# Kernel tuning notes

Measured on AMD Instinct MI355X. Metric: run time of the kernel, lower is better.

The kernel has to match this reference:

```python
import jax, jax.numpy as jnp
import numpy as np

NUM_HEADS = 32
NUM_KV_HEADS = 8
HEAD_DIM = 128
SCALE = 1.0 / np.sqrt(HEAD_DIM)
BATCH = 16
MAX_CTX = 2048
NUM_SLOTS = BATCH * MAX_CTX + BATCH  # 32784; last BATCH slots are the write targets


def setup_inputs() -> dict:
    key = jax.random.key(0)
    ks = jax.random.split(key, 8)
    q = jax.random.normal(ks[0], (BATCH, NUM_HEADS, HEAD_DIM), dtype=jnp.float32)
    k = jax.random.normal(ks[1], (BATCH, NUM_KV_HEADS, HEAD_DIM), dtype=jnp.float32)
    v = jax.random.normal(ks[2], (BATCH, NUM_KV_HEADS, HEAD_DIM), dtype=jnp.float32)
    k_cache = jax.random.normal(ks[3], (NUM_SLOTS, NUM_KV_HEADS, HEAD_DIM), dtype=jnp.float32)
    v_cache = jax.random.normal(ks[4], (NUM_SLOTS, NUM_KV_HEADS, HEAD_DIM), dtype=jnp.float32)
    # each decode token writes its new kv into a fresh slot at the end of the pool
    slot_mapping = (BATCH * MAX_CTX + jnp.arange(BATCH)).astype(jnp.int64)
    # sparse-controller-selected active slots per request (paged, irregular)
    active_slots = jax.random.randint(ks[5], (BATCH, MAX_CTX), 0, NUM_SLOTS).astype(jnp.int64)
    # make the current token's slot the last active slot of its own request
    active_slots = active_slots.at[:, -1].set(slot_mapping)
    context_lens = jax.random.randint(ks[6], (BATCH,), 1, MAX_CTX + 1).astype(jnp.int64)
    return {
        "q": q, "k": k, "v": v,
        "k_cache": k_cache, "v_cache": v_cache,
        "slot_mapping": slot_mapping,
        "active_slots": active_slots,
        "context_lens": context_lens,
    }


def _attend(q, k, v, k_cache, v_cache, slot_mapping, active_slots, context_lens):
    # store_kvcache: scatter new k/v into flat slot cache; slot == -1 is skipped
    safe_slots = jnp.where(slot_mapping < 0, NUM_SLOTS, slot_mapping)  # OOB -> dropped
    kc = k_cache.at[safe_slots].set(k, mode="drop")
    vc = v_cache.at[safe_slots].set(v, mode="drop")

    # paged gather of the per-request active KV pages
    K = kc[active_slots]  # [B, L, Hkv, D]
    V = vc[active_slots]  # [B, L, Hkv, D]

    B, H, D = q.shape
    G = H // NUM_KV_HEADS  # GQA group size
    qg = q.reshape(B, NUM_KV_HEADS, G, D)

    # flash-decode stage1+stage2 == numerically-stable softmax attention over active slots
    scores = jnp.einsum("bkgd,blkd->bkgl", qg, K) * SCALE  # [B, Hkv, G, L]
    valid = jnp.arange(active_slots.shape[1])[None, :] < context_lens[:, None]  # [B, L]
    scores = jnp.where(valid[:, None, None, :], scores, jnp.float32(-1e30))
    p = jax.nn.softmax(scores, axis=-1)
    o = jnp.einsum("bkgl,blkd->bkgd", p, V).reshape(B, H, D)
    return o


def reference(q, k, v, k_cache, v_cache, slot_mapping, active_slots, context_lens):
    return _attend(q, k, v, k_cache, v_cache, slot_mapping, active_slots, context_lens)
```

## Files before the change

kernel.cpp:

```cpp
#include <hip/hip_runtime.h>
#include <hip/hip_bf16.h>
#include <float.h>

#define B 16
#define H 32
#define HKV 8
#define G 4
#define D 128
#define LMAX 2048
#define SCALE 0.08838834764831844f

template <int CHUNK>
__global__ __launch_bounds__(64, 3) void attn_partial(
    const float* __restrict__ q,
    const float* __restrict__ kin,
    const float* __restrict__ vin,
    const float* __restrict__ kc,
    const float* __restrict__ vc,
    const int*  __restrict__ slot_mapping,
    const int*  __restrict__ active_slots,
    const int*  __restrict__ context_lens,
    float* __restrict__ part_o,
    float* __restrict__ part_ml)
{
    constexpr int NSPLIT = LMAX / CHUNK;
    const int tid   = threadIdx.x;
    const int split = blockIdx.x % NSPLIT;
    const int h     = (blockIdx.x / NSPLIT) % HKV;
    const int b     = blockIdx.x / (NSPLIT * HKV);

    const int ctx   = context_lens[b];
    const int start = split * CHUNK;
    int nvalid = ctx - start;
    if (nvalid > CHUNK) nvalid = CHUNK;

    const size_t pbase = ((size_t)(b * HKV + h) * NSPLIT + split) * G;

    if (nvalid <= 0) {
        if (tid < G * 2) part_ml[pbase * 2 + tid] = (tid & 1) ? 0.f : -FLT_MAX;
        return;
    }

    __shared__ const float* kp[CHUNK];
    __shared__ const float* vp[CHUNK];
    __shared__ float4 sc4[CHUNK];

    for (int li = tid; li < nvalid; li += 64) {
        const int s = active_slots[b * LMAX + start + li];
        int ov = -1;
#pragma unroll
        for (int j = 0; j < 16; ++j)
            if (slot_mapping[j] == s) ov = j;
        kp[li] = (ov >= 0) ? kin + ((size_t)ov * HKV + h) * D : kc + ((size_t)s * HKV + h) * D;
        vp[li] = (ov >= 0) ? vin + ((size_t)ov * HKV + h) * D : vc + ((size_t)s * HKV + h) * D;
    }

    const int grp   = tid >> 3;
    const int lane8 = tid & 7;

    float4 qv[G][4];
#pragma unroll
    for (int g = 0; g < G; ++g) {
        const float* qp = q + ((size_t)(b * H + h * G + g)) * D;
#pragma unroll
        for (int i = 0; i < 4; ++i) {
            float4 t = *(const float4*)(qp + i * 32 + lane8 * 4);
            qv[g][i] = make_float4(t.x * SCALE, t.y * SCALE, t.z * SCALE, t.w * SCALE);
        }
    }

    constexpr int KIT = CHUNK / 8;
#pragma unroll 2
    for (int it = 0; it < KIT; ++it) {
        const int r  = it * 8 + grp;
        const int rl = (r < nvalid) ? r : nvalid - 1;
        const float* kb = kp[rl];
        float pd0 = 0.f, pd1 = 0.f, pd2 = 0.f, pd3 = 0.f;
#pragma unroll
        for (int j = 0; j < 4; ++j) {
            const float4 kv = *(const float4*)(kb + j * 32 + lane8 * 4);
            pd0 += kv.x * qv[0][j].x + kv.y * qv[0][j].y + kv.z * qv[0][j].z + kv.w * qv[0][j].w;
            pd1 += kv.x * qv[1][j].x + kv.y * qv[1][j].y + kv.z * qv[1][j].z + kv.w * qv[1][j].w;
            pd2 += kv.x * qv[2][j].x + kv.y * qv[2][j].y + kv.z * qv[2][j].z + kv.w * qv[2][j].w;
            pd3 += kv.x * qv[3][j].x + kv.y * qv[3][j].y + kv.z * qv[3][j].z + kv.w * qv[3][j].w;
        }
#pragma unroll
        for (int msk = 1; msk < 8; msk <<= 1) {
            pd0 += __shfl_xor(pd0, msk, 8);
            pd1 += __shfl_xor(pd1, msk, 8);
            pd2 += __shfl_xor(pd2, msk, 8);
            pd3 += __shfl_xor(pd3, msk, 8);
        }
        if (lane8 == 0) sc4[r] = make_float4(pd0, pd1, pd2, pd3);
    }

    {
        constexpr int SR = (CHUNK + 63) / 64;
        float4 s[SR];
#pragma unroll
        for (int k2 = 0; k2 < SR; ++k2) {
            const int l = tid + k2 * 64;
            s[k2] = sc4[l];
            if (l >= nvalid) s[k2] = make_float4(-1e30f, -1e30f, -1e30f, -1e30f);
        }
        float m0 = s[0].x, m1 = s[0].y, m2 = s[0].z, m3 = s[0].w;
#pragma unroll
        for (int k2 = 1; k2 < SR; ++k2) {
            m0 = fmaxf(m0, s[k2].x); m1 = fmaxf(m1, s[k2].y);
            m2 = fmaxf(m2, s[k2].z); m3 = fmaxf(m3, s[k2].w);
        }
#pragma unroll
        for (int msk = 1; msk < 64; msk <<= 1) {
            m0 = fmaxf(m0, __shfl_xor(m0, msk));
            m1 = fmaxf(m1, __shfl_xor(m1, msk));
            m2 = fmaxf(m2, __shfl_xor(m2, msk));
            m3 = fmaxf(m3, __shfl_xor(m3, msk));
        }
        float l0 = 0.f, l1 = 0.f, l2 = 0.f, l3 = 0.f;
#pragma unroll
        for (int k2 = 0; k2 < SR; ++k2) {
            const float4 p = make_float4(__expf(s[k2].x - m0), __expf(s[k2].y - m1),
                                         __expf(s[k2].z - m2), __expf(s[k2].w - m3));
            l0 += p.x; l1 += p.y; l2 += p.z; l3 += p.w;
            sc4[tid + k2 * 64] = p;
        }
#pragma unroll
        for (int msk = 1; msk < 64; msk <<= 1) {
            l0 += __shfl_xor(l0, msk);
            l1 += __shfl_xor(l1, msk);
            l2 += __shfl_xor(l2, msk);
            l3 += __shfl_xor(l3, msk);
        }
        if (tid == 0) {
            *(float4*)&part_ml[pbase * 2 + 0] = make_float4(m0, l0, m1, l1);
            *(float4*)&part_ml[pbase * 2 + 4] = make_float4(m2, l2, m3, l3);
        }
    }

    {
        const int half = tid >> 5;
        const int dl   = tid & 31;
        float4 a0 = {0,0,0,0}, a1 = {0,0,0,0}, a2 = {0,0,0,0}, a3 = {0,0,0,0};
        constexpr int VJ = CHUNK / 2;
#pragma unroll 4
        for (int j = 0; j < VJ; ++j) {
            const int r  = 2 * j + half;
            const int rl = (r < nvalid) ? r : nvalid - 1;
            const float4 vv = *(const float4*)(vp[rl] + dl * 4);
            const float4 p4 = sc4[r];
            a0.x += p4.x * vv.x; a0.y += p4.x * vv.y; a0.z += p4.x * vv.z; a0.w += p4.x * vv.w;
            a1.x += p4.y * vv.x; a1.y += p4.y * vv.y; a1.z += p4.y * vv.z; a1.w += p4.y * vv.w;
            a2.x += p4.z * vv.x; a2.y += p4.z * vv.y; a2.z += p4.z * vv.z; a2.w += p4.z * vv.w;
            a3.x += p4.w * vv.x; a3.y += p4.w * vv.y; a3.z += p4.w * vv.z; a3.w += p4.w * vv.w;
        }
#pragma unroll
        for (int c = 0; c < 4; ++c) {
            ((float*)&a0)[c] += __shfl_xor(((float*)&a0)[c], 32);
            ((float*)&a1)[c] += __shfl_xor(((float*)&a1)[c], 32);
            ((float*)&a2)[c] += __shfl_xor(((float*)&a2)[c], 32);
            ((float*)&a3)[c] += __shfl_xor(((float*)&a3)[c], 32);
        }
        if (half == 0) {
            *(float4*)(part_o + (pbase + 0) * D + dl * 4) = a0;
            *(float4*)(part_o + (pbase + 1) * D + dl * 4) = a1;
        } else {
            *(float4*)(part_o + (pbase + 2) * D + dl * 4) = a2;
            *(float4*)(part_o + (pbase + 3) * D + dl * 4) = a3;
        }
    }
}

__global__ __launch_bounds__(128) void attn_reduce(
    const float* __restrict__ part_o,
    const float* __restrict__ part_ml,
    float* __restrict__ out,
    int nsplit)
{
    const int g = blockIdx.x & 3;
    const int h = (blockIdx.x >> 2) & 7;
    const int b = blockIdx.x >> 5;
    const int d = threadIdx.x;

    __shared__ float mlds[32], llds[32];
    const size_t base = (size_t)(b * HKV + h) * nsplit;

    for (int s = d; s < nsplit; s += 128) {
        mlds[s] = part_ml[((base + s) * G + g) * 2 + 0];
        llds[s] = part_ml[((base + s) * G + g) * 2 + 1];
    }
    __syncthreads();

    float M = -FLT_MAX;
    for (int s = 0; s < nsplit; ++s)
        if (llds[s] > 0.f) M = fmaxf(M, mlds[s]);

    float L = 0.f, acc = 0.f;
    for (int s = 0; s < nsplit; ++s) {
        const float l = llds[s];
        if (l > 0.f) {
            const float e = __expf(mlds[s] - M);
            L += l * e;
            acc += e * part_o[((base + s) * G + g) * D + d];
        }
    }
    out[((size_t)(b * H) + h * G + g) * D + d] = acc / (L > 0.f ? L : 1.f);
}

extern "C" void kernel_launch(void* const* d_in, const int* in_sizes, int n_in,
                              void* d_out, int out_size, void* d_ws, size_t ws_size,
                              hipStream_t stream) {
    const float* q  = (const float*)d_in[0];
    const float* k  = (const float*)d_in[1];
    const float* v  = (const float*)d_in[2];
    const float* kc = (const float*)d_in[3];
    const float* vc = (const float*)d_in[4];
    const int* slot_mapping = (const int*)d_in[5];
    const int* active_slots = (const int*)d_in[6];
    const int* context_lens = (const int*)d_in[7];
    float* out = (float*)d_out;

    const size_t perSplit = (size_t)B * HKV * (G * D + G * 2) * sizeof(float);
    int nsplit = 8;
    if (ws_size >= 32 * perSplit)      nsplit = 32;
    else if (ws_size >= 16 * perSplit) nsplit = 16;

    float* part_o  = (float*)d_ws;
    float* part_ml = part_o + (size_t)B * HKV * nsplit * G * D;

    if (nsplit == 32) {
        attn_partial<64><<<B * HKV * 32, 64, 0, stream>>>(
            q, k, v, kc, vc, slot_mapping, active_slots, context_lens, part_o, part_ml);
    } else if (nsplit == 16) {
        attn_partial<128><<<B * HKV * 16, 64, 0, stream>>>(
            q, k, v, kc, vc, slot_mapping, active_slots, context_lens, part_o, part_ml);
    } else {
        attn_partial<256><<<B * HKV * 8, 64, 0, stream>>>(
            q, k, v, kc, vc, slot_mapping, active_slots, context_lens, part_o, part_ml);
    }
    attn_reduce<<<B * HKV * G, 128, 0, stream>>>(part_o, part_ml, out, nsplit);
}
```

Before: 41.82 us.

## Fuse QK and PV into single-pass online softmax with lazy rescaling

Replaces the three-phase partial kernel (scores to LDS, block softmax, separate PV pass) with one loop in which each 8-lane group loads K and V rows together and keeps an online softmax with a lazy-rescale threshold. The eight group partials are merged through shared memory at the end. The reduce kernel is widened to 256 threads and splits the nsplit loop across two halves. The intent is to overlap K and V gathers and drop the serial phases, at the cost of many more accumulator registers (64 floats of output per thread). The launch-bounds occupancy hint is also removed.

```diff
diff --git a/kernel.cpp b/kernel.cpp
--- a/kernel.cpp
+++ b/kernel.cpp
@@ -9,9 +9,10 @@
 #define D 128
 #define LMAX 2048
 #define SCALE 0.08838834764831844f
+#define THR 8.0f
 
 template <int CHUNK>
-__global__ __launch_bounds__(64, 3) void attn_partial(
+__global__ __launch_bounds__(64) void attn_partial(
     const float* __restrict__ q,
     const float* __restrict__ kin,
     const float* __restrict__ vin,
@@ -43,14 +44,18 @@
 
     __shared__ const float* kp[CHUNK];
     __shared__ const float* vp[CHUNK];
-    __shared__ float4 sc4[CHUNK];
-
+    __shared__ float  red[8][G][D];
+    __shared__ float2 mlred[8][G];
+
+    int smv[16];
+#pragma unroll
+    for (int j = 0; j < 16; ++j) smv[j] = slot_mapping[j];
     for (int li = tid; li < nvalid; li += 64) {
         const int s = active_slots[b * LMAX + start + li];
         int ov = -1;
 #pragma unroll
         for (int j = 0; j < 16; ++j)
-            if (slot_mapping[j] == s) ov = j;
+            if (smv[j] == s) ov = j;
         kp[li] = (ov >= 0) ? kin + ((size_t)ov * HKV + h) * D : kc + ((size_t)s * HKV + h) * D;
         vp[li] = (ov >= 0) ? vin + ((size_t)ov * HKV + h) * D : vc + ((size_t)s * HKV + h) * D;
     }
@@ -63,26 +68,36 @@
     for (int g = 0; g < G; ++g) {
         const float* qp = q + ((size_t)(b * H + h * G + g)) * D;
 #pragma unroll
-        for (int i = 0; i < 4; ++i) {
-            float4 t = *(const float4*)(qp + i * 32 + lane8 * 4);
-            qv[g][i] = make_float4(t.x * SCALE, t.y * SCALE, t.z * SCALE, t.w * SCALE);
-        }
-    }
-
-    constexpr int KIT = CHUNK / 8;
+        for (int j = 0; j < 4; ++j) {
+            float4 t = *(const float4*)(qp + j * 32 + lane8 * 4);
+            qv[g][j] = make_float4(t.x * SCALE, t.y * SCALE, t.z * SCALE, t.w * SCALE);
+        }
+    }
+
+    float m0 = -1e30f, m1 = -1e30f, m2 = -1e30f, m3 = -1e30f;
+    float l0 = 0.f, l1 = 0.f, l2 = 0.f, l3 = 0.f;
+    float4 o0[4] = {}, o1[4] = {}, o2[4] = {}, o3[4] = {};
+
+    constexpr int ITERS = CHUNK / 8;
 #pragma unroll 2
-    for (int it = 0; it < KIT; ++it) {
+    for (int it = 0; it < ITERS; ++it) {
         const int r  = it * 8 + grp;
         const int rl = (r < nvalid) ? r : nvalid - 1;
         const float* kb = kp[rl];
+        const float* vb = vp[rl];
+        float4 kv[4], vv[4];
+#pragma unroll
+        for (int j = 0; j < 4; ++j) kv[j] = *(const float4*)(kb + j * 32 + lane8 * 4);
+#pragma unroll
+        for (int j = 0; j < 4; ++j) vv[j] = *(const float4*)(vb + j * 32 + lane8 * 4);
+
         float pd0 = 0.f, pd1 = 0.f, pd2 = 0.f, pd3 = 0.f;
 #pragma unroll
         for (int j = 0; j < 4; ++j) {
-            const float4 kv = *(const float4*)(kb + j * 32 + lane8 * 4);
-            pd0 += kv.x * qv[0][j].x + kv.y * qv[0][j].y + kv.z * qv[0][j].z + kv.w * qv[0][j].w;
-            pd1 += kv.x * qv[1][j].x + kv.y * qv[1][j].y + kv.z * qv[1][j].z + kv.w * qv[1][j].w;
-            pd2 += kv.x * qv[2][j].x + kv.y * qv[2][j].y + kv.z * qv[2][j].z + kv.w * qv[2][j].w;
-            pd3 += kv.x * qv[3][j].x + kv.y * qv[3][j].y + kv.z * qv[3][j].z + kv.w * qv[3][j].w;
+            pd0 += kv[j].x * qv[0][j].x + kv[j].y * qv[0][j].y + kv[j].z * qv[0][j].z + kv[j].w * qv[0][j].w;
+            pd1 += kv[j].x * qv[1][j].x + kv[j].y * qv[1][j].y + kv[j].z * qv[1][j].z + kv[j].w * qv[1][j].w;
+            pd2 += kv[j].x * qv[2][j].x + kv[j].y * qv[2][j].y + kv[j].z * qv[2][j].z + kv[j].w * qv[2][j].w;
+            pd3 += kv[j].x * qv[3][j].x + kv[j].y * qv[3][j].y + kv[j].z * qv[3][j].z + kv[j].w * qv[3][j].w;
         }
 #pragma unroll
         for (int msk = 1; msk < 8; msk <<= 1) {
@@ -91,86 +106,87 @@
             pd2 += __shfl_xor(pd2, msk, 8);
             pd3 += __shfl_xor(pd3, msk, 8);
         }
-        if (lane8 == 0) sc4[r] = make_float4(pd0, pd1, pd2, pd3);
-    }
-
-    {
-        constexpr int SR = (CHUNK + 63) / 64;
-        float4 s[SR];
-#pragma unroll
-        for (int k2 = 0; k2 < SR; ++k2) {
-            const int l = tid + k2 * 64;
-            s[k2] = sc4[l];
-            if (l >= nvalid) s[k2] = make_float4(-1e30f, -1e30f, -1e30f, -1e30f);
-        }
-        float m0 = s[0].x, m1 = s[0].y, m2 = s[0].z, m3 = s[0].w;
-#pragma unroll
-        for (int k2 = 1; k2 < SR; ++k2) {
-            m0 = fmaxf(m0, s[k2].x); m1 = fmaxf(m1, s[k2].y);
-            m2 = fmaxf(m2, s[k2].z); m3 = fmaxf(m3, s[k2].w);
-        }
-#pragma unroll
-        for (int msk = 1; msk < 64; msk <<= 1) {
-            m0 = fmaxf(m0, __shfl_xor(m0, msk));
-            m1 = fmaxf(m1, __shfl_xor(m1, msk));
-            m2 = fmaxf(m2, __shfl_xor(m2, msk));
-            m3 = fmaxf(m3, __shfl_xor(m3, msk));
-        }
-        float l0 = 0.f, l1 = 0.f, l2 = 0.f, l3 = 0.f;
-#pragma unroll
-        for (int k2 = 0; k2 < SR; ++k2) {
-            const float4 p = make_float4(__expf(s[k2].x - m0), __expf(s[k2].y - m1),
-                                         __expf(s[k2].z - m2), __expf(s[k2].w - m3));
-            l0 += p.x; l1 += p.y; l2 += p.z; l3 += p.w;
-            sc4[tid + k2 * 64] = p;
-        }
-#pragma unroll
-        for (int msk = 1; msk < 64; msk <<= 1) {
-            l0 += __shfl_xor(l0, msk);
-            l1 += __shfl_xor(l1, msk);
-            l2 += __shfl_xor(l2, msk);
-            l3 += __shfl_xor(l3, msk);
-        }
+
+        const bool valid = (r < nvalid);
+        const float s0 = valid ? pd0 : -1e30f;
+        const float s1 = valid ? pd1 : -1e30f;
+        const float s2 = valid ? pd2 : -1e30f;
+        const float s3 = valid ? pd3 : -1e30f;
+
+        if (s0 > m0 + THR) {
+            const float sc = __expf(m0 - s0); l0 *= sc; m0 = s0;
+#pragma unroll
+            for (int j = 0; j < 4; ++j) { o0[j].x *= sc; o0[j].y *= sc; o0[j].z *= sc; o0[j].w *= sc; }
+        }
+        if (s1 > m1 + THR) {
+            const float sc = __expf(m1 - s1); l1 *= sc; m1 = s1;
+#pragma unroll
+            for (int j = 0; j < 4; ++j) { o1[j].x *= sc; o1[j].y *= sc; o1[j].z *= sc; o1[j].w *= sc; }
+        }
+        if (s2 > m2 + THR) {
+            const float sc = __expf(m2 - s2); l2 *= sc; m2 = s2;
+#pragma unroll
+            for (int j = 0; j < 4; ++j) { o2[j].x *= sc; o2[j].y *= sc; o2[j].z *= sc; o2[j].w *= sc; }
+        }
+        if (s3 > m3 + THR) {
+            const float sc = __expf(m3 - s3); l3 *= sc; m3 = s3;
+#pragma unroll
+            for (int j = 0; j < 4; ++j) { o3[j].x *= sc; o3[j].y *= sc; o3[j].z *= sc; o3[j].w *= sc; }
+        }
+
+        const float p0 = __expf(s0 - m0);
+        const float p1 = __expf(s1 - m1);
+        const float p2 = __expf(s2 - m2);
+        const float p3 = __expf(s3 - m3);
+        l0 += p0; l1 += p1; l2 += p2; l3 += p3;
+#pragma unroll
+        for (int j = 0; j < 4; ++j) {
+            o0[j].x += p0 * vv[j].x; o0[j].y += p0 * vv[j].y; o0[j].z += p0 * vv[j].z; o0[j].w += p0 * vv[j].w;
+            o1[j].x += p1 * vv[j].x; o1[j].y += p1 * vv[j].y; o1[j].z += p1 * vv[j].z; o1[j].w += p1 * vv[j].w;
+            o2[j].x += p2 * vv[j].x; o2[j].y += p2 * vv[j].y; o2[j].z += p2 * vv[j].z; o2[j].w += p2 * vv[j].w;
+            o3[j].x += p3 * vv[j].x; o3[j].y += p3 * vv[j].y; o3[j].z += p3 * vv[j].z; o3[j].w += p3 * vv[j].w;
+        }
+    }
+
+#pragma unroll
+    for (int j = 0; j < 4; ++j) {
+        *(float4*)&red[grp][0][j * 32 + lane8 * 4] = o0[j];
+        *(float4*)&red[grp][1][j * 32 + lane8 * 4] = o1[j];
+        *(float4*)&red[grp][2][j * 32 + lane8 * 4] = o2[j];
+        *(float4*)&red[grp][3][j * 32 + lane8 * 4] = o3[j];
+    }
+    if (lane8 == 0) {
+        mlred[grp][0] = make_float2(m0, l0);
+        mlred[grp][1] = make_float2(m1, l1);
+        mlred[grp][2] = make_float2(m2, l2);
+        mlred[grp][3] = make_float2(m3, l3);
+    }
+    __syncthreads();
+
+#pragma unroll
+    for (int g = 0; g < G; ++g) {
+        float Mg = -1e30f;
+#pragma unroll
+        for (int gr = 0; gr < 8; ++gr) Mg = fmaxf(Mg, mlred[gr][g].x);
+        float Lg = 0.f, acc0 = 0.f, acc1 = 0.f;
+#pragma unroll
+        for (int gr = 0; gr < 8; ++gr) {
+            const float2 ml = mlred[gr][g];
+            const float w = __expf(ml.x - Mg);
+            Lg += ml.y * w;
+            acc0 += red[gr][g][tid]      * w;
+            acc1 += red[gr][g][tid + 64] * w;
+        }
+        part_o[(pbase + g) * D + tid]      = acc0;
+        part_o[(pbase + g) * D + tid + 64] = acc1;
         if (tid == 0) {
-            *(float4*)&part_ml[pbase * 2 + 0] = make_float4(m0, l0, m1, l1);
-            *(float4*)&part_ml[pbase * 2 + 4] = make_float4(m2, l2, m3, l3);
-        }
-    }
-
-    {
-        const int half = tid >> 5;
-        const int dl   = tid & 31;
-        float4 a0 = {0,0,0,0}, a1 = {0,0,0,0}, a2 = {0,0,0,0}, a3 = {0,0,0,0};
-        constexpr int VJ = CHUNK / 2;
-#pragma unroll 4
-        for (int j = 0; j < VJ; ++j) {
-            const int r  = 2 * j + half;
-            const int rl = (r < nvalid) ? r : nvalid - 1;
-            const float4 vv = *(const float4*)(vp[rl] + dl * 4);
-            const float4 p4 = sc4[r];
-            a0.x += p4.x * vv.x; a0.y += p4.x * vv.y; a0.z += p4.x * vv.z; a0.w += p4.x * vv.w;
-            a1.x += p4.y * vv.x; a1.y += p4.y * vv.y; a1.z += p4.y * vv.z; a1.w += p4.y * vv.w;
-            a2.x += p4.z * vv.x; a2.y += p4.z * vv.y; a2.z += p4.z * vv.z; a2.w += p4.z * vv.w;
-            a3.x += p4.w * vv.x; a3.y += p4.w * vv.y; a3.z += p4.w * vv.z; a3.w += p4.w * vv.w;
-        }
-#pragma unroll
-        for (int c = 0; c < 4; ++c) {
-            ((float*)&a0)[c] += __shfl_xor(((float*)&a0)[c], 32);
-            ((float*)&a1)[c] += __shfl_xor(((float*)&a1)[c], 32);
-            ((float*)&a2)[c] += __shfl_xor(((float*)&a2)[c], 32);
-            ((float*)&a3)[c] += __shfl_xor(((float*)&a3)[c], 32);
-        }
-        if (half == 0) {
-            *(float4*)(part_o + (pbase + 0) * D + dl * 4) = a0;
-            *(float4*)(part_o + (pbase + 1) * D + dl * 4) = a1;
-        } else {
-            *(float4*)(part_o + (pbase + 2) * D + dl * 4) = a2;
-            *(float4*)(part_o + (pbase + 3) * D + dl * 4) = a3;
+            part_ml[(pbase + g) * 2 + 0] = Mg;
+            part_ml[(pbase + g) * 2 + 1] = Lg;
         }
     }
 }
 
-__global__ __launch_bounds__(128) void attn_reduce(
+__global__ __launch_bounds__(256) void attn_reduce(
     const float* __restrict__ part_o,
     const float* __restrict__ part_ml,
     float* __restrict__ out,
@@ -179,12 +195,15 @@
     const int g = blockIdx.x & 3;
     const int h = (blockIdx.x >> 2) & 7;
     const int b = blockIdx.x >> 5;
-    const int d = threadIdx.x;
-
-    __shared__ float mlds[32], llds[32];
+    const int d  = threadIdx.x & 127;
+    const int sp = threadIdx.x >> 7;
+
+    __shared__ float mlds[64], llds[64];
+    __shared__ float red[128];
+    __shared__ float lred;
     const size_t base = (size_t)(b * HKV + h) * nsplit;
 
-    for (int s = d; s < nsplit; s += 128) {
+    for (int s = threadIdx.x; s < nsplit; s += 256) {
         mlds[s] = part_ml[((base + s) * G + g) * 2 + 0];
         llds[s] = part_ml[((base + s) * G + g) * 2 + 1];
     }
@@ -195,7 +214,7 @@
         if (llds[s] > 0.f) M = fmaxf(M, mlds[s]);
 
     float L = 0.f, acc = 0.f;
-    for (int s = 0; s < nsplit; ++s) {
+    for (int s = sp; s < nsplit; s += 2) {
         const float l = llds[s];
         if (l > 0.f) {
             const float e = __expf(mlds[s] - M);
@@ -203,7 +222,16 @@
             acc += e * part_o[((base + s) * G + g) * D + d];
         }
     }
-    out[((size_t)(b * H) + h * G + g) * D + d] = acc / (L > 0.f ? L : 1.f);
+    if (sp == 1) {
+        red[d] = acc;
+        if (d == 0) lred = L;
+    }
+    __syncthreads();
+    if (sp == 0) {
+        acc += red[d];
+        L   += lred;
+        out[((size_t)(b * H) + h * G + g) * D + d] = acc / (L > 0.f ? L : 1.f);
+    }
 }
 
 extern "C" void kernel_launch(void* const* d_in, const int* in_sizes, int n_in,
@@ -237,5 +265,5 @@
         attn_partial<256><<<B * HKV * 8, 64, 0, stream>>>(
             q, k, v, kc, vc, slot_mapping, active_slots, context_lens, part_o, part_ml);
     }
-    attn_reduce<<<B * HKV * G, 128, 0, stream>>>(part_o, part_ml, out, nsplit);
+    attn_reduce<<<B * HKV * G, 256, 0, stream>>>(part_o, part_ml, out, nsplit);
 }
```

New measurement: 42.09 us. No clear change (+0.6%).
